# Performance work log

Measured on AMD Instinct MI355X. Metric: run time of the kernel, lower is better.

The kernel has to match this reference:

```python
import jax, jax.numpy as jnp
import numpy as np

B, L, HEAD_IN, DIM = 16, 512, 4, 64
HEAD_OUT = 4


def setup_inputs() -> dict:
    key = jax.random.key(0)
    k1, k2 = jax.random.split(key)
    inp = jax.random.normal(k1, (B, L, HEAD_IN, DIM), dtype=jnp.float32)
    # one (dim x dim) 'general' attention weight per (head_out, head_in) pair
    W = jax.random.normal(k2, (HEAD_OUT, HEAD_IN, DIM, DIM), dtype=jnp.float32) / np.sqrt(DIM)
    return {"inp": inp, "W": W}


def reference(inp, W):
    # inp: [b, l, j(head_in), d]; W: [o(head_out), j, d, e]
    b, l, j, d = inp.shape
    scale = 1.0 / jnp.sqrt(jnp.asarray(d, inp.dtype))
    # q_ij = x_j @ W_ij  -> [o, j, b, l, e]
    q = jnp.einsum('bljd,ojde->ojble', inp, W)
    # scores_ij = q_ij @ x_j^T / sqrt(d) -> [o, j, b, l, m]
    scores = jnp.einsum('ojble,bmje->ojblm', q, inp) * scale
    attn = jax.nn.softmax(scores, axis=-1)          # [o, j, b, l, m]
    ctx = jnp.einsum('ojblm,bmjd->ojbld', attn, inp)  # [o, j, b, l, d]
    out = jnp.mean(ctx, axis=1)                      # mean over head_in -> [o, b, l, d]
    out = jnp.transpose(out, (1, 2, 0, 3))           # [b, l, head_out, d]
    return out, attn
```

## Files before the change

kernel.cpp:

```cpp
#include <hip/hip_runtime.h>
#include <stdint.h>


typedef __bf16 bf16x8 __attribute__((ext_vector_type(8)));
typedef float  f32x4  __attribute__((ext_vector_type(4)));
typedef unsigned int u32;
typedef u32 u32x4 __attribute__((ext_vector_type(4)));

#define XB_OFF  0
#define WT_OFF  65536
#define QB_OFF  73728
#define P3B_OFF 65536
#define LDS_BYTES 77824

static __device__ __forceinline__ u32 f2bf(float f) {
    u32 u = __builtin_bit_cast(u32, f);
    u += 0x7fffu + ((u >> 16) & 1u);
    return u >> 16;
}
static __device__ __forceinline__ float bflo2f(u32 p) { return __builtin_bit_cast(float, p << 16); }
static __device__ __forceinline__ float bfhi2f(u32 p) { return __builtin_bit_cast(float, p & 0xffff0000u); }

__global__ __launch_bounds__(256, 2) void convattn_kernel(
    const float* __restrict__ inp,
    const float* __restrict__ Wg,
    float* __restrict__ out)
{
    extern __shared__ __align__(16) char smem[];
    const int tid  = threadIdx.x;
    const int wave = tid >> 6;
    const int lane = tid & 63;
    const int g    = lane >> 4;
    const int ln   = lane & 15;
    const int rl   = lane >> 2;
    const int rq   = lane & 3;

    const int bid = blockIdx.x;
    const int b  = bid & 15;
    const int o  = (bid >> 4) & 3;
    const int lt = bid >> 6;
    const int l0 = lt * 64 + wave * 16;

    float* attn_out = out + (size_t)2097152;
    char* qb  = smem + QB_OFF  + wave * 1024;
    char* p3b = smem + P3B_OFF + wave * 1280;

    const int sq = tid & 15;
    const int sp = tid >> 4;

    f32x4 acc_c[4];
    #pragma unroll
    for (int i = 0; i < 4; ++i) { f32x4 z = {0.f,0.f,0.f,0.f}; acc_c[i] = z; }

    #pragma unroll 1
    for (int j = 0; j < 4; ++j) {
        __syncthreads();

        {
            const int e0 = sq << 2;
            #pragma unroll
            for (int it = 0; it < 16; ++it) {
                const int m0 = it * 32 + sp * 2;
                const float* src = inp + (((size_t)b * 512 + m0) * 4 + j) * 64 + e0;
                const float4 va = *(const float4*)src;
                const float4 vb = *(const float4*)(src + 256);
                uint2 w0; w0.x = f2bf(va.x) | (f2bf(va.y) << 16); w0.y = f2bf(va.z) | (f2bf(va.w) << 16);
                *(uint2*)(smem + XB_OFF + m0 * 128 + (((sq >> 1) ^ (m0 & 7)) * 16) + ((sq & 1) * 8)) = w0;
                uint2 w1; w1.x = f2bf(vb.x) | (f2bf(vb.y) << 16); w1.y = f2bf(vb.z) | (f2bf(vb.w) << 16);
                *(uint2*)(smem + XB_OFF + (m0 + 1) * 128 + (((sq >> 1) ^ ((m0 + 1) & 7)) * 16) + ((sq & 1) * 8)) = w1;
            }
            const int wd = tid >> 2;
            const int we = (tid & 3) << 4;
            const float* wsrc = Wg + (((size_t)o * 4 + j) * 64 + wd) * 64 + we;
            #pragma unroll
            for (int c = 0; c < 4; ++c) {
                const float4 wv = *(const float4*)(wsrc + c * 4);
                const int e = we + c * 4;
                const u32 q0 = f2bf(wv.x), q1 = f2bf(wv.y), q2 = f2bf(wv.z), q3 = f2bf(wv.w);
                *(unsigned short*)(smem + WT_OFF + (e + 0) * 128 + (((wd >> 3) ^ ((e + 0) & 7)) * 16) + ((wd & 7) * 2)) = (unsigned short)q0;
                *(unsigned short*)(smem + WT_OFF + (e + 1) * 128 + (((wd >> 3) ^ ((e + 1) & 7)) * 16) + ((wd & 7) * 2)) = (unsigned short)q1;
                *(unsigned short*)(smem + WT_OFF + (e + 2) * 128 + (((wd >> 3) ^ ((e + 2) & 7)) * 16) + ((wd & 7) * 2)) = (unsigned short)q2;
                *(unsigned short*)(smem + WT_OFF + (e + 3) * 128 + (((wd >> 3) ^ ((e + 3) & 7)) * 16) + ((wd & 7) * 2)) = (unsigned short)q3;
            }
        }
        __syncthreads();

        bf16x8 bq0, bq1;
        {
            const int lq = l0 + ln;
            const bf16x8 aq0 = *(const bf16x8*)(smem + XB_OFF + lq * 128 + ((g ^ (lq & 7)) * 16));
            const bf16x8 aq1 = *(const bf16x8*)(smem + XB_OFF + lq * 128 + (((4 + g) ^ (lq & 7)) * 16));
            #pragma unroll
            for (int h = 0; h < 2; ++h) {
                #pragma unroll
                for (int et = 0; et < 2; ++et) {
                    const int e = h * 32 + et * 16 + ln;
                    const bf16x8 bw0 = *(const bf16x8*)(smem + WT_OFF + e * 128 + ((g ^ (e & 7)) * 16));
                    const bf16x8 bw1 = *(const bf16x8*)(smem + WT_OFF + e * 128 + (((4 + g) ^ (e & 7)) * 16));
                    f32x4 t = {0.f,0.f,0.f,0.f};
                    t = __builtin_amdgcn_mfma_f32_16x16x32_bf16(aq0, bw0, t, 0, 0, 0);
                    t = __builtin_amdgcn_mfma_f32_16x16x32_bf16(aq1, bw1, t, 0, 0, 0);
                    const int cell = et * 2 + (ln >> 3);
                    #pragma unroll
                    for (int r = 0; r < 4; ++r) {
                        const int lr = g * 4 + r;
                        *(unsigned short*)(qb + lr * 64 + ((cell ^ (lr & 3)) * 16) + ((ln & 7) * 2)) = (unsigned short)f2bf(t[r]);
                    }
                }
                const bf16x8 bq = *(const bf16x8*)(qb + ln * 64 + ((g ^ (ln & 3)) * 16));
                if (h == 0) bq0 = bq; else bq1 = bq;
                __builtin_amdgcn_sched_barrier(0);
            }
        }

        float sum = 0.f;
        u32 sLo[32], sHi[32];
        #pragma unroll
        for (int mt = 0; mt < 32; ++mt) {
            const int m = mt * 16 + ln;
            const bf16x8 ax0 = *(const bf16x8*)(smem + XB_OFF + m * 128 + ((g ^ (m & 7)) * 16));
            const bf16x8 ax1 = *(const bf16x8*)(smem + XB_OFF + m * 128 + (((4 + g) ^ (m & 7)) * 16));
            f32x4 t = {0.f,0.f,0.f,0.f};
            t = __builtin_amdgcn_mfma_f32_16x16x32_bf16(ax0, bq0, t, 0, 0, 0);
            t = __builtin_amdgcn_mfma_f32_16x16x32_bf16(ax1, bq1, t, 0, 0, 0);
            const float e0v = __expf(t[0] * 0.125f);
            const float e1v = __expf(t[1] * 0.125f);
            const float e2v = __expf(t[2] * 0.125f);
            const float e3v = __expf(t[3] * 0.125f);
            sum += (e0v + e1v) + (e2v + e3v);
            sLo[mt] = f2bf(e0v) | (f2bf(e1v) << 16);
            sHi[mt] = f2bf(e2v) | (f2bf(e3v) << 16);
        }
        sum += __shfl_xor(sum, 16, 64);
        sum += __shfl_xor(sum, 32, 64);
        const float inv = 1.0f / sum;

        __syncthreads();

        {
            const int e0 = sq << 2;
            #pragma unroll
            for (int it = 0; it < 16; ++it) {
                const int m0 = it * 32 + sp * 2;
                const float* src = inp + (((size_t)b * 512 + m0) * 4 + j) * 64 + e0;
                const float4 va = *(const float4*)src;
                const float4 vb = *(const float4*)(src + 256);
                const u32 p0 = f2bf(va.x) | (f2bf(vb.x) << 16);
                const u32 p1 = f2bf(va.y) | (f2bf(vb.y) << 16);
                const u32 p2 = f2bf(va.z) | (f2bf(vb.z) << 16);
                const u32 p3v = f2bf(va.w) | (f2bf(vb.w) << 16);
                const u32 pc[4] = {p0, p1, p2, p3v};
                #pragma unroll
                for (int c = 0; c < 4; ++c) {
                    const int d = e0 + c;
                    *(u32*)(smem + XB_OFF + d * 1024 + (((m0 >> 3) ^ ((d >> 2) & 7)) * 16) + ((m0 & 7) * 2)) = pc[c];
                }
            }
        }
        __syncthreads();

        const size_t abase = ((size_t)((o * 4 + j) * 16 + b)) * 262144 + (size_t)l0 * 512;
        const int srcLo = ((g & 1) << 5) + ln;
        const int srcHi = srcLo + 16;
        #pragma unroll
        for (int ch = 0; ch < 16; ++ch) {
            u32 pLo[2], pHi[2];
            #pragma unroll
            for (int s = 0; s < 2; ++s) {
                const int mt = ch * 2 + s;
                const float a0v = bflo2f(sLo[mt]) * inv;
                const float a1v = bfhi2f(sLo[mt]) * inv;
                const float a2v = bflo2f(sHi[mt]) * inv;
                const float a3v = bfhi2f(sHi[mt]) * inv;
                *(float*)(p3b + ln * 80 + (g * 4 + 0) * 4) = a0v;
                *(float*)(p3b + ln * 80 + (g * 4 + 1) * 4) = a1v;
                *(float*)(p3b + ln * 80 + (g * 4 + 2) * 4) = a2v;
                *(float*)(p3b + ln * 80 + (g * 4 + 3) * 4) = a3v;
                const f32x4 rv = *(const f32x4*)(p3b + rl * 80 + rq * 16);
                __builtin_nontemporal_store(rv,
                    (f32x4*)(attn_out + abase + (size_t)rl * 512 + mt * 16 + rq * 4));
                pLo[s] = f2bf(a0v) | (f2bf(a1v) << 16);
                pHi[s] = f2bf(a2v) | (f2bf(a3v) << 16);
            }
            const u32 a0s = (u32)__shfl((int)pLo[0], srcLo, 64);
            const u32 a1s = (u32)__shfl((int)pHi[0], srcLo, 64);
            const u32 a2s = (u32)__shfl((int)pLo[0], srcHi, 64);
            const u32 a3s = (u32)__shfl((int)pHi[0], srcHi, 64);
            const u32 b0s = (u32)__shfl((int)pLo[1], srcLo, 64);
            const u32 b1s = (u32)__shfl((int)pHi[1], srcLo, 64);
            const u32 b2s = (u32)__shfl((int)pLo[1], srcHi, 64);
            const u32 b3s = (u32)__shfl((int)pHi[1], srcHi, 64);
            const bool hi = (g >= 2);
            const u32 dw0 = hi ? b0s : a0s;
            const u32 dw1 = hi ? b1s : a1s;
            const u32 dw2 = hi ? b2s : a2s;
            const u32 dw3 = hi ? b3s : a3s;
            const bf16x8 bfrag = __builtin_bit_cast(bf16x8, (u32x4){dw0, dw1, dw2, dw3});
            #pragma unroll
            for (int dt = 0; dt < 4; ++dt) {
                const int d = dt * 16 + ln;
                const bf16x8 ax = *(const bf16x8*)(smem + XB_OFF + d * 1024 +
                                   (((ch * 4 + g) ^ ((d >> 2) & 7)) * 16));
                acc_c[dt] = __builtin_amdgcn_mfma_f32_16x16x32_bf16(ax, bfrag, acc_c[dt], 0, 0, 0);
            }
        }
    }

    #pragma unroll
    for (int dt = 0; dt < 4; ++dt) {
        #pragma unroll
        for (int r = 0; r < 4; ++r)
            *(float*)(p3b + ln * 80 + (g * 4 + r) * 4) = acc_c[dt][r] * 0.25f;
        const f32x4 rv = *(const f32x4*)(p3b + rl * 80 + rq * 16);
        *(f32x4*)(out + (((size_t)b * 512 + (l0 + rl)) * 4 + o) * 64 + dt * 16 + rq * 4) = rv;
    }
}

extern "C" void kernel_launch(void* const* d_in, const int* in_sizes, int n_in,
                              void* d_out, int out_size, void* d_ws, size_t ws_size,
                              hipStream_t stream) {
    const float* inp = (const float*)d_in[0];
    const float* Wg  = (const float*)d_in[1];
    float* out = (float*)d_out;
    (void)hipFuncSetAttribute((const void*)convattn_kernel,
                              hipFuncAttributeMaxDynamicSharedMemorySize, LDS_BYTES);
    convattn_kernel<<<dim3(512), dim3(256), LDS_BYTES, stream>>>(inp, Wg, out);
}
```

Measured before the change: 409.2 us.

## Split head_in across blocks with 8-wave blocks and atomic output reduction

Each block now has 8 waves covering 128 query rows and handles only two of the four head_in slices. Blocks for the two halves combine the mean over head_in by atomically adding into a zeroed output, which needs a memset before launch. The LDS transposes for the attention and output stores are removed in favour of direct per-lane vector stores. This spreads the same work over more waves per block and reuses each staged x tile across more rows, at the cost of atomics, an extra memset, and less coalesced attention stores.

```diff
diff --git a/kernel.cpp b/kernel.cpp
--- a/kernel.cpp
+++ b/kernel.cpp
@@ -10,7 +10,6 @@
 #define XB_OFF  0
 #define WT_OFF  65536
 #define QB_OFF  73728
-#define P3B_OFF 65536
 #define LDS_BYTES 77824
 
 static __device__ __forceinline__ u32 f2bf(float f) {
@@ -21,7 +20,7 @@
 static __device__ __forceinline__ float bflo2f(u32 p) { return __builtin_bit_cast(float, p << 16); }
 static __device__ __forceinline__ float bfhi2f(u32 p) { return __builtin_bit_cast(float, p & 0xffff0000u); }
 
-__global__ __launch_bounds__(256, 2) void convattn_kernel(
+__global__ __launch_bounds__(512, 4) void convattn_kernel(
     const float* __restrict__ inp,
     const float* __restrict__ Wg,
     float* __restrict__ out)
@@ -32,18 +31,16 @@
     const int lane = tid & 63;
     const int g    = lane >> 4;
     const int ln   = lane & 15;
-    const int rl   = lane >> 2;
-    const int rq   = lane & 3;
 
     const int bid = blockIdx.x;
     const int b  = bid & 15;
     const int o  = (bid >> 4) & 3;
-    const int lt = bid >> 6;
-    const int l0 = lt * 64 + wave * 16;
+    const int lt = (bid >> 6) & 3;
+    const int jh = bid >> 8;
+    const int l0 = lt * 128 + wave * 16;
 
     float* attn_out = out + (size_t)2097152;
-    char* qb  = smem + QB_OFF  + wave * 1024;
-    char* p3b = smem + P3B_OFF + wave * 1280;
+    char* qb = smem + QB_OFF + wave * 512;
 
     const int sq = tid & 15;
     const int sp = tid >> 4;
@@ -53,14 +50,15 @@
     for (int i = 0; i < 4; ++i) { f32x4 z = {0.f,0.f,0.f,0.f}; acc_c[i] = z; }
 
     #pragma unroll 1
-    for (int j = 0; j < 4; ++j) {
+    for (int jj = 0; jj < 2; ++jj) {
+        const int j = jh * 2 + jj;
         __syncthreads();
 
         {
             const int e0 = sq << 2;
             #pragma unroll
-            for (int it = 0; it < 16; ++it) {
-                const int m0 = it * 32 + sp * 2;
+            for (int it = 0; it < 8; ++it) {
+                const int m0 = it * 64 + sp * 2;
                 const float* src = inp + (((size_t)b * 512 + m0) * 4 + j) * 64 + e0;
                 const float4 va = *(const float4*)src;
                 const float4 vb = *(const float4*)(src + 256);
@@ -69,11 +67,11 @@
                 uint2 w1; w1.x = f2bf(vb.x) | (f2bf(vb.y) << 16); w1.y = f2bf(vb.z) | (f2bf(vb.w) << 16);
                 *(uint2*)(smem + XB_OFF + (m0 + 1) * 128 + (((sq >> 1) ^ ((m0 + 1) & 7)) * 16) + ((sq & 1) * 8)) = w1;
             }
-            const int wd = tid >> 2;
-            const int we = (tid & 3) << 4;
+            const int wd = tid >> 3;
+            const int we = (tid & 7) << 3;
             const float* wsrc = Wg + (((size_t)o * 4 + j) * 64 + wd) * 64 + we;
             #pragma unroll
-            for (int c = 0; c < 4; ++c) {
+            for (int c = 0; c < 2; ++c) {
                 const float4 wv = *(const float4*)(wsrc + c * 4);
                 const int e = we + c * 4;
                 const u32 q0 = f2bf(wv.x), q1 = f2bf(wv.y), q2 = f2bf(wv.z), q3 = f2bf(wv.w);
@@ -90,27 +88,23 @@
             const int lq = l0 + ln;
             const bf16x8 aq0 = *(const bf16x8*)(smem + XB_OFF + lq * 128 + ((g ^ (lq & 7)) * 16));
             const bf16x8 aq1 = *(const bf16x8*)(smem + XB_OFF + lq * 128 + (((4 + g) ^ (lq & 7)) * 16));
-            #pragma unroll
-            for (int h = 0; h < 2; ++h) {
+            bf16x8 rd[4];
+            #pragma unroll
+            for (int h = 0; h < 4; ++h) {
+                const int e = h * 16 + ln;
+                const bf16x8 bw0 = *(const bf16x8*)(smem + WT_OFF + e * 128 + ((g ^ (e & 7)) * 16));
+                const bf16x8 bw1 = *(const bf16x8*)(smem + WT_OFF + e * 128 + (((4 + g) ^ (e & 7)) * 16));
+                f32x4 t = {0.f,0.f,0.f,0.f};
+                t = __builtin_amdgcn_mfma_f32_16x16x32_bf16(aq0, bw0, t, 0, 0, 0);
+                t = __builtin_amdgcn_mfma_f32_16x16x32_bf16(aq1, bw1, t, 0, 0, 0);
                 #pragma unroll
-                for (int et = 0; et < 2; ++et) {
-                    const int e = h * 32 + et * 16 + ln;
-                    const bf16x8 bw0 = *(const bf16x8*)(smem + WT_OFF + e * 128 + ((g ^ (e & 7)) * 16));
-                    const bf16x8 bw1 = *(const bf16x8*)(smem + WT_OFF + e * 128 + (((4 + g) ^ (e & 7)) * 16));
-                    f32x4 t = {0.f,0.f,0.f,0.f};
-                    t = __builtin_amdgcn_mfma_f32_16x16x32_bf16(aq0, bw0, t, 0, 0, 0);
-                    t = __builtin_amdgcn_mfma_f32_16x16x32_bf16(aq1, bw1, t, 0, 0, 0);
-                    const int cell = et * 2 + (ln >> 3);
-                    #pragma unroll
-                    for (int r = 0; r < 4; ++r) {
-                        const int lr = g * 4 + r;
-                        *(unsigned short*)(qb + lr * 64 + ((cell ^ (lr & 3)) * 16) + ((ln & 7) * 2)) = (unsigned short)f2bf(t[r]);
-                    }
-                }
-                const bf16x8 bq = *(const bf16x8*)(qb + ln * 64 + ((g ^ (ln & 3)) * 16));
-                if (h == 0) bq0 = bq; else bq1 = bq;
+                for (int r = 0; r < 4; ++r)
+                    *(unsigned short*)(qb + (g * 4 + r) * 32 + ln * 2) = (unsigned short)f2bf(t[r]);
+                rd[h] = *(const bf16x8*)(qb + ln * 32 + (g & 1) * 16);
                 __builtin_amdgcn_sched_barrier(0);
             }
+            bq0 = (g < 2) ? rd[0] : rd[1];
+            bq1 = (g < 2) ? rd[2] : rd[3];
         }
 
         float sum = 0.f;
@@ -140,8 +134,8 @@
         {
             const int e0 = sq << 2;
             #pragma unroll
-            for (int it = 0; it < 16; ++it) {
-                const int m0 = it * 32 + sp * 2;
+            for (int it = 0; it < 8; ++it) {
+                const int m0 = it * 64 + sp * 2;
                 const float* src = inp + (((size_t)b * 512 + m0) * 4 + j) * 64 + e0;
                 const float4 va = *(const float4*)src;
                 const float4 vb = *(const float4*)(src + 256);
@@ -159,7 +153,7 @@
         }
         __syncthreads();
 
-        const size_t abase = ((size_t)((o * 4 + j) * 16 + b)) * 262144 + (size_t)l0 * 512;
+        const size_t abase = ((size_t)((o * 4 + j) * 16 + b)) * 262144 + (size_t)(l0 + ln) * 512;
         const int srcLo = ((g & 1) << 5) + ln;
         const int srcHi = srcLo + 16;
         #pragma unroll
@@ -172,13 +166,8 @@
                 const float a1v = bfhi2f(sLo[mt]) * inv;
                 const float a2v = bflo2f(sHi[mt]) * inv;
                 const float a3v = bfhi2f(sHi[mt]) * inv;
-                *(float*)(p3b + ln * 80 + (g * 4 + 0) * 4) = a0v;
-                *(float*)(p3b + ln * 80 + (g * 4 + 1) * 4) = a1v;
-                *(float*)(p3b + ln * 80 + (g * 4 + 2) * 4) = a2v;
-                *(float*)(p3b + ln * 80 + (g * 4 + 3) * 4) = a3v;
-                const f32x4 rv = *(const f32x4*)(p3b + rl * 80 + rq * 16);
-                __builtin_nontemporal_store(rv,
-                    (f32x4*)(attn_out + abase + (size_t)rl * 512 + mt * 16 + rq * 4));
+                const f32x4 av = {a0v, a1v, a2v, a3v};
+                *(f32x4*)(attn_out + abase + mt * 16 + g * 4) = av;
                 pLo[s] = f2bf(a0v) | (f2bf(a1v) << 16);
                 pHi[s] = f2bf(a2v) | (f2bf(a3v) << 16);
             }
@@ -206,13 +195,12 @@
         }
     }
 
+    float* obase = out + (((size_t)b * 512 + (l0 + ln)) * 4 + o) * 64;
     #pragma unroll
     for (int dt = 0; dt < 4; ++dt) {
         #pragma unroll
         for (int r = 0; r < 4; ++r)
-            *(float*)(p3b + ln * 80 + (g * 4 + r) * 4) = acc_c[dt][r] * 0.25f;
-        const f32x4 rv = *(const f32x4*)(p3b + rl * 80 + rq * 16);
-        *(f32x4*)(out + (((size_t)b * 512 + (l0 + rl)) * 4 + o) * 64 + dt * 16 + rq * 4) = rv;
+            unsafeAtomicAdd(obase + dt * 16 + g * 4 + r, acc_c[dt][r] * 0.25f);
     }
 }
 
@@ -222,7 +210,8 @@
     const float* inp = (const float*)d_in[0];
     const float* Wg  = (const float*)d_in[1];
     float* out = (float*)d_out;
+    (void)hipMemsetAsync(d_out, 0, (size_t)2097152 * sizeof(float), stream);
     (void)hipFuncSetAttribute((const void*)convattn_kernel,
                               hipFuncAttributeMaxDynamicSharedMemorySize, LDS_BYTES);
-    convattn_kernel<<<dim3(512), dim3(256), LDS_BYTES, stream>>>(inp, Wg, out);
+    convattn_kernel<<<dim3(512), dim3(512), LDS_BYTES, stream>>>(inp, Wg, out);
 }
```

Result: slower. 506.6 us (+23.8%).
